# Performance work log

Hardware: AMD Instinct MI355X
Metric: run time of the kernel (lower is better)

The kernel has to match this reference:

```python
import jax, jax.numpy as jnp
import numpy as np
import math

B, S, D, H = 4, 2048, 1024, 16
DK = D // H
DFF = 1024  # FeedForward default d_ff=1024 (DecoderLayer passes only d_model)
EPS = 1e-6
SQRT_2_OVER_PI = math.sqrt(2.0 / math.pi)


def setup_inputs() -> dict:
    key = jax.random.key(0)
    ks = jax.random.split(key, 12)
    sc = 0.02
    x = jax.random.normal(ks[0], (B, S, D), dtype=jnp.float32)
    # causal look-ahead mask: 1 where attendable, 0 where masked
    mask = jnp.broadcast_to(jnp.tril(jnp.ones((S, S), dtype=jnp.int32)), (B, S, S))
    inp = {
        'x': x,
        'mask': mask,
        'Wq': jax.random.normal(ks[1], (D, D), jnp.float32) * sc,
        'bq': jnp.zeros((D,), jnp.float32),
        'Wk': jax.random.normal(ks[2], (D, D), jnp.float32) * sc,
        'bk': jnp.zeros((D,), jnp.float32),
        'Wv': jax.random.normal(ks[3], (D, D), jnp.float32) * sc,
        'bv': jnp.zeros((D,), jnp.float32),
        'Wo': jax.random.normal(ks[4], (D, D), jnp.float32) * sc,
        'bo': jnp.zeros((D,), jnp.float32),
        'W1': jax.random.normal(ks[5], (D, DFF), jnp.float32) * sc,
        'b1': jnp.zeros((DFF,), jnp.float32),
        'W2': jax.random.normal(ks[6], (DFF, D), jnp.float32) * sc,
        'b2': jnp.zeros((D,), jnp.float32),
        'alpha1': jnp.ones((D,), jnp.float32),
        'bias1': jnp.zeros((D,), jnp.float32),
        'alpha2': jnp.ones((D,), jnp.float32),
        'bias2': jnp.zeros((D,), jnp.float32),
    }
    return inp


def _norm(x, alpha, bias):
    # torch: (x - mean) / (x.std(unbiased=True) + eps) * alpha + bias
    mean = jnp.mean(x, axis=-1, keepdims=True)
    var = jnp.sum((x - mean) ** 2, axis=-1, keepdims=True) / (x.shape[-1] - 1)
    std = jnp.sqrt(var)
    return alpha * (x - mean) / (std + EPS) + bias


def _gelu(x):
    return 0.5 * x * (1.0 + jnp.tanh(SQRT_2_OVER_PI * (x + 0.044715 * x ** 3)))


def reference(x, mask, Wq, bq, Wk, bk, Wv, bv, Wo, bo, W1, b1, W2, b2,
              alpha1, bias1, alpha2, bias2):
    b, s, d = x.shape
    x2 = _norm(x, alpha1, bias1)
    q = (x2 @ Wq + bq).reshape(b, s, H, DK).transpose(0, 2, 1, 3)  # bhsd
    k = (x2 @ Wk + bk).reshape(b, s, H, DK).transpose(0, 2, 1, 3)
    v = (x2 @ Wv + bv).reshape(b, s, H, DK).transpose(0, 2, 1, 3)
    scores = jnp.einsum('bhqd,bhkd->bhqk', q, k) / jnp.sqrt(jnp.float32(DK))
    scores = jnp.where(mask[:, None, :, :] == 0, jnp.float32(-1e9), scores)
    probs = jax.nn.softmax(scores, axis=-1)
    attn = jnp.einsum('bhqk,bhkd->bhqd', probs, v)
    concat = attn.transpose(0, 2, 1, 3).reshape(b, s, d)
    x = x + (concat @ Wo + bo)
    x2 = _norm(x, alpha2, bias2)
    ff = _gelu(x2 @ W1 + b1) @ W2 + b2
    return x + ff
```

## Files before the change

### kernel.cpp

```cpp
#include <hip/hip_runtime.h>
#include <hip/hip_bf16.h>
#include <math.h>


#define B_ 4
#define S_ 2048
#define D_ 1024
#define H_ 16
#define DFF_ 1024

typedef __attribute__((ext_vector_type(8))) short short8;
typedef __attribute__((ext_vector_type(8))) unsigned short ushort8;
typedef __attribute__((ext_vector_type(4))) float f32x4;

__device__ __forceinline__ unsigned short f2bf(float f) {
  __hip_bfloat16 h = __float2bfloat16(f);
  return *reinterpret_cast<unsigned short*>(&h);
}

__device__ __forceinline__ void gload16(const void* g, void* l) {
  __builtin_amdgcn_global_load_lds(
      (const __attribute__((address_space(1))) void*)g,
      (__attribute__((address_space(3))) void*)l, 16, 0, 0);
}

__global__ __launch_bounds__(256) void tcast6_k(
    const float* s0, const float* s1, const float* s2, const float* s3,
    const float* s4, const float* s5, unsigned short* d0, unsigned short* d1,
    unsigned short* d2, unsigned short* d3, unsigned short* d4,
    unsigned short* d5) {
  const float* src;
  unsigned short* dst;
  switch (blockIdx.z) {
    case 0: src = s0; dst = d0; break;
    case 1: src = s1; dst = d1; break;
    case 2: src = s2; dst = d2; break;
    case 3: src = s3; dst = d3; break;
    case 4: src = s4; dst = d4; break;
    default: src = s5; dst = d5; break;
  }
  __shared__ float tile[64][65];
  const int k0 = blockIdx.y * 64, n0 = blockIdx.x * 64;
  const int t = threadIdx.x;
  const int r = t >> 2, c0 = (t & 3) * 16;
  const float4* sp =
      reinterpret_cast<const float4*>(src + (size_t)(k0 + r) * 1024 + n0 + c0);
#pragma unroll
  for (int j = 0; j < 4; ++j) {
    float4 v = sp[j];
    tile[r][c0 + 4 * j] = v.x;
    tile[r][c0 + 4 * j + 1] = v.y;
    tile[r][c0 + 4 * j + 2] = v.z;
    tile[r][c0 + 4 * j + 3] = v.w;
  }
  __syncthreads();
  ushort8 o0, o1;
#pragma unroll
  for (int j = 0; j < 8; ++j) o0[j] = f2bf(tile[c0 + j][r]);
#pragma unroll
  for (int j = 0; j < 8; ++j) o1[j] = f2bf(tile[c0 + 8 + j][r]);
  unsigned short* dp = dst + (size_t)(n0 + r) * 1024 + k0 + c0;
  *reinterpret_cast<ushort8*>(dp) = o0;
  *reinterpret_cast<ushort8*>(dp + 8) = o1;
}

__global__ __launch_bounds__(256) void ln_k(const float* __restrict__ x,
                                            const float* __restrict__ alpha,
                                            const float* __restrict__ bias,
                                            unsigned short* __restrict__ out) {
  int row = blockIdx.x, t = threadIdx.x;
  float4 v = reinterpret_cast<const float4*>(x + (size_t)row * D_)[t];
  float s = v.x + v.y + v.z + v.w;
  float q = v.x * v.x + v.y * v.y + v.z * v.z + v.w * v.w;
#pragma unroll
  for (int off = 32; off > 0; off >>= 1) {
    s += __shfl_down(s, off);
    q += __shfl_down(q, off);
  }
  __shared__ float ss[4], sq[4], stat[2];
  if ((t & 63) == 0) { ss[t >> 6] = s; sq[t >> 6] = q; }
  __syncthreads();
  if (t == 0) {
    float S = ss[0] + ss[1] + ss[2] + ss[3];
    float Q = sq[0] + sq[1] + sq[2] + sq[3];
    float mean = S * (1.0f / D_);
    float var = fmaxf((Q - D_ * mean * mean) * (1.0f / (D_ - 1)), 0.0f);
    stat[0] = mean;
    stat[1] = 1.0f / (sqrtf(var) + 1e-6f);
  }
  __syncthreads();
  float mean = stat[0], inv = stat[1];
  float4 a = reinterpret_cast<const float4*>(alpha)[t];
  float4 b = reinterpret_cast<const float4*>(bias)[t];
  ushort4 o;
  o.x = f2bf((v.x - mean) * inv * a.x + b.x);
  o.y = f2bf((v.y - mean) * inv * a.y + b.y);
  o.z = f2bf((v.z - mean) * inv * a.z + b.z);
  o.w = f2bf((v.w - mean) * inv * a.w + b.w);
  reinterpret_cast<ushort4*>(out + (size_t)row * D_)[t] = o;
}

__device__ __forceinline__ void gemm_core64(
    const unsigned short* __restrict__ A, const unsigned short* __restrict__ Wt,
    int m0, int n0, int K, unsigned short* As ,
    unsigned short* Bs , f32x4 (&acc)[2][4]) {
  const int t = threadIdx.x;
  const int wv = t >> 6, lane = t & 63, quad = lane >> 4, l16 = lane & 15;
  const int wm = wv >> 1, wn = wv & 1;
  const int lr8 = lane >> 3;
  const int lseg = ((lane & 7) ^ lr8) * 8;

  const unsigned short* Ag0 = A + (size_t)(m0 + wv * 16 + lr8) * K + lseg;
  const unsigned short* Ag1 = A + (size_t)(m0 + wv * 16 + 8 + lr8) * K + lseg;
  const unsigned short* Bg0 = Wt + (size_t)(n0 + wv * 32 + lr8) * K + lseg;
  const unsigned short* Bg1 = Wt + (size_t)(n0 + wv * 32 + 8 + lr8) * K + lseg;
  const unsigned short* Bg2 = Wt + (size_t)(n0 + wv * 32 + 16 + lr8) * K + lseg;
  const unsigned short* Bg3 = Wt + (size_t)(n0 + wv * 32 + 24 + lr8) * K + lseg;
  unsigned short* Al0 = &As[(wv * 16) * 64];
  unsigned short* Al1 = &As[(wv * 16 + 8) * 64];
  unsigned short* Bl0 = &Bs[(wv * 32) * 64];
  unsigned short* Bl1 = &Bs[(wv * 32 + 8) * 64];
  unsigned short* Bl2 = &Bs[(wv * 32 + 16) * 64];
  unsigned short* Bl3 = &Bs[(wv * 32 + 24) * 64];

  for (int k0 = 0; k0 < K; k0 += 64) {
    gload16(Ag0, Al0);
    gload16(Ag1, Al1);
    gload16(Bg0, Bl0);
    gload16(Bg1, Bl1);
    gload16(Bg2, Bl2);
    gload16(Bg3, Bl3);
    __syncthreads();
    short8 af[2][2], bf[2][4];
#pragma unroll
    for (int p = 0; p < 2; ++p) {
#pragma unroll
      for (int mt = 0; mt < 2; ++mt) {
        int r = wm * 32 + mt * 16 + l16;
        af[p][mt] = *reinterpret_cast<const short8*>(
            &As[r * 64 + (((p * 4 + quad) ^ (r & 7)) << 3)]);
      }
#pragma unroll
      for (int nt = 0; nt < 4; ++nt) {
        int r = wn * 64 + nt * 16 + l16;
        bf[p][nt] = *reinterpret_cast<const short8*>(
            &Bs[r * 64 + (((p * 4 + quad) ^ (r & 7)) << 3)]);
      }
    }
#pragma unroll
    for (int p = 0; p < 2; ++p)
#pragma unroll
      for (int mt = 0; mt < 2; ++mt)
#pragma unroll
        for (int nt = 0; nt < 4; ++nt)
          acc[mt][nt] = __builtin_amdgcn_mfma_f32_16x16x32_bf16(
              af[p][mt], bf[p][nt], acc[mt][nt], 0, 0, 0);
    __syncthreads();
    Ag0 += 64; Ag1 += 64; Bg0 += 64; Bg1 += 64; Bg2 += 64; Bg3 += 64;
  }
}

__global__ __launch_bounds__(256, 4) void gemm_k(
    const unsigned short* __restrict__ A, const unsigned short* __restrict__ Wt,
    const float* __restrict__ bias, const float* __restrict__ res,
    void* __restrict__ outp, int M, int N, int K, int flags) {
  __shared__ unsigned short As[64 * 64];
  __shared__ unsigned short Bs[128 * 64];
  const int t = threadIdx.x;
  const int m0 = blockIdx.y * 64, n0 = blockIdx.x * 128;
  const int wv = t >> 6, lane = t & 63, quad = lane >> 4, l16 = lane & 15;
  const int wm = wv >> 1, wn = wv & 1;
  f32x4 acc[2][4] = {};
  gemm_core64(A, Wt, m0, n0, K, As, Bs, acc);

  const bool obf = flags & 1, dog = flags & 2;
#pragma unroll
  for (int nt = 0; nt < 4; ++nt) {
    int col = n0 + wn * 64 + nt * 16 + l16;
    float bv = bias[col];
#pragma unroll
    for (int mt = 0; mt < 2; ++mt) {
#pragma unroll
      for (int r = 0; r < 4; ++r) {
        int row = m0 + wm * 32 + mt * 16 + quad * 4 + r;
        float v = acc[mt][nt][r] + bv;
        if (res) v += res[(size_t)row * N + col];
        if (dog) {
          float e = __expf(1.5957691216057308f * (v + 0.044715f * v * v * v));
          float th = 1.0f - 2.0f / (1.0f + e);
          v = 0.5f * v * (1.0f + th);
        }
        if (obf)
          ((unsigned short*)outp)[(size_t)row * N + col] = f2bf(v);
        else
          ((float*)outp)[(size_t)row * N + col] = v;
      }
    }
  }
}

__global__ __launch_bounds__(256, 4) void gemmqkv_k(
    const unsigned short* __restrict__ A, const unsigned short* __restrict__ Wt,
    const float* __restrict__ bq, const float* __restrict__ bk,
    const float* __restrict__ bv, unsigned short* __restrict__ outq,
    unsigned short* __restrict__ outk, unsigned short* __restrict__ outvt,
    int M, int K) {
  __shared__ unsigned short As[64 * 64];
  __shared__ unsigned short Bs[128 * 64];
  const int t = threadIdx.x;
  const int m0 = blockIdx.y * 64, n0 = blockIdx.x * 128;
  const int wv = t >> 6, lane = t & 63, quad = lane >> 4, l16 = lane & 15;
  const int wm = wv >> 1, wn = wv & 1;
  f32x4 acc[2][4] = {};
  gemm_core64(A, Wt, m0, n0, K, As, Bs, acc);

  const int seg = n0 >> 10;
  const int nb = n0 & 1023;
  const float* bias = (seg == 0) ? bq : (seg == 1) ? bk : bv;
  if (seg < 2) {
    unsigned short* o = (seg == 0) ? outq : outk;
#pragma unroll
    for (int nt = 0; nt < 4; ++nt) {
      int col = nb + wn * 64 + nt * 16 + l16;
      float bvv = bias[col];
#pragma unroll
      for (int mt = 0; mt < 2; ++mt)
#pragma unroll
        for (int r = 0; r < 4; ++r) {
          int row = m0 + wm * 32 + mt * 16 + quad * 4 + r;
          o[(size_t)row * D_ + col] = f2bf(acc[mt][nt][r] + bvv);
        }
    }
  } else {
#pragma unroll
    for (int nt = 0; nt < 4; ++nt) {
      int col = nb + wn * 64 + nt * 16 + l16;
      float bvv = bias[col];
      int h = col >> 6, dk = col & 63;
#pragma unroll
      for (int mt = 0; mt < 2; ++mt) {
        int m = m0 + wm * 32 + mt * 16 + quad * 4;
        int b = m >> 11, sidx = m & 2047;
        ushort4 o;
        o.x = f2bf(acc[mt][nt][0] + bvv);
        o.y = f2bf(acc[mt][nt][1] + bvv);
        o.z = f2bf(acc[mt][nt][2] + bvv);
        o.w = f2bf(acc[mt][nt][3] + bvv);
        *reinterpret_cast<ushort4*>(
            &outvt[(((size_t)(b * 16 + h) * 64 + dk) * 2048 + sidx)]) = o;
      }
    }
  }
}

__global__ __launch_bounds__(256, 2) void attn_k(
    const unsigned short* __restrict__ Q, const unsigned short* __restrict__ Kg,
    const unsigned short* __restrict__ VT, unsigned short* __restrict__ Og) {
  __shared__ unsigned short Ks[64 * 64];
  __shared__ unsigned short Vs[64 * 64];
  __shared__ unsigned short Ps[4 * 32 * 72];
  const int t = threadIdx.x;
  const int pair = blockIdx.x >> 6, bh = blockIdx.x & 63;
  const int b = bh >> 4, h = bh & 15;
  const int hi = 31 - pair, lo = pair;
  const int w = t >> 6, lane = t & 63, quad = lane >> 4, l16 = lane & 15;
  const int qhi0 = hi * 64 + w * 16, qlo0 = lo * 64 + w * 16;
  unsigned short* PsW = &Ps[w * 32 * 72];

  short8 qfh[2], qfl[2];
#pragma unroll
  for (int kc = 0; kc < 2; ++kc) {
    qfh[kc] = *reinterpret_cast<const short8*>(
        Q + (size_t)(b * S_ + qhi0 + l16) * D_ + h * 64 + kc * 32 + quad * 8);
    qfl[kc] = *reinterpret_cast<const short8*>(
        Q + (size_t)(b * S_ + qlo0 + l16) * D_ + h * 64 + kc * 32 + quad * 8);
  }
  f32x4 Oh[4] = {}, Ol[4] = {};
  float lh_acc = 0.0f, ll_acc = 0.0f;

  const int srA = w * 8 + (lane >> 3);
  const int ssA = ((lane & 7) ^ (srA & 7)) * 8;
  const int srB = srA + 32;
  const int ssB = ((lane & 7) ^ (srB & 7)) * 8;
  const unsigned short* KgA = Kg + (size_t)(b * S_ + srA) * D_ + h * 64 + ssA;
  const unsigned short* KgB = Kg + (size_t)(b * S_ + srB) * D_ + h * 64 + ssB;
  const unsigned short* VgA = VT + ((size_t)bh * 64 + srA) * 2048 + ssA;
  const unsigned short* VgB = VT + ((size_t)bh * 64 + srB) * 2048 + ssB;
  unsigned short* KlA = &Ks[(w * 8) * 64];
  unsigned short* KlB = &Ks[(32 + w * 8) * 64];
  unsigned short* VlA = &Vs[(w * 8) * 64];
  unsigned short* VlB = &Vs[(32 + w * 8) * 64];

  const float C0 = 0.18033688011f;
  const float C1 = -23.08312065f;

  for (int kt = 0; kt <= hi; ++kt) {
    const int k0 = kt * 64;
    const bool dolo = (kt <= lo);

    gload16(KgA, KlA);
    gload16(KgB, KlB);
    gload16(VgA, VlA);
    gload16(VgB, VlB);
    __syncthreads();

    f32x4 sch[4] = {}, scl[4] = {};
#pragma unroll
    for (int mt = 0; mt < 4; ++mt) {
      int r = mt * 16 + l16;
      short8 kf0 = *reinterpret_cast<const short8*>(
          &Ks[r * 64 + ((quad ^ (r & 7)) << 3)]);
      short8 kf1 = *reinterpret_cast<const short8*>(
          &Ks[r * 64 + (((4 + quad) ^ (r & 7)) << 3)]);
      sch[mt] = __builtin_amdgcn_mfma_f32_16x16x32_bf16(kf0, qfh[0], sch[mt],
                                                        0, 0, 0);
      sch[mt] = __builtin_amdgcn_mfma_f32_16x16x32_bf16(kf1, qfh[1], sch[mt],
                                                        0, 0, 0);
      if (dolo) {
        scl[mt] = __builtin_amdgcn_mfma_f32_16x16x32_bf16(kf0, qfl[0], scl[mt],
                                                          0, 0, 0);
        scl[mt] = __builtin_amdgcn_mfma_f32_16x16x32_bf16(kf1, qfl[1], scl[mt],
                                                          0, 0, 0);
      }
    }

    {
      const bool diag = (kt == hi);
      const int q = qhi0 + l16;
#pragma unroll
      for (int mt = 0; mt < 4; ++mt) {
        float pv[4];
#pragma unroll
        for (int r = 0; r < 4; ++r) {
          int key = k0 + mt * 16 + quad * 4 + r;
          float p = __builtin_amdgcn_exp2f(fmaf(sch[mt][r], C0, C1));
          if (diag && key > q) p = 0.0f;
          lh_acc += p;
          pv[r] = p;
        }
        ushort4 pk = {f2bf(pv[0]), f2bf(pv[1]), f2bf(pv[2]), f2bf(pv[3])};
        *reinterpret_cast<ushort4*>(&PsW[l16 * 72 + mt * 16 + quad * 4]) = pk;
      }
    }
    if (dolo) {
      const bool diag = (kt == lo);
      const int q = qlo0 + l16;
#pragma unroll
      for (int mt = 0; mt < 4; ++mt) {
        float pv[4];
#pragma unroll
        for (int r = 0; r < 4; ++r) {
          int key = k0 + mt * 16 + quad * 4 + r;
          float p = __builtin_amdgcn_exp2f(fmaf(scl[mt][r], C0, C1));
          if (diag && key > q) p = 0.0f;
          ll_acc += p;
          pv[r] = p;
        }
        ushort4 pk = {f2bf(pv[0]), f2bf(pv[1]), f2bf(pv[2]), f2bf(pv[3])};
        *reinterpret_cast<ushort4*>(
            &PsW[(16 + l16) * 72 + mt * 16 + quad * 4]) = pk;
      }
    }
    __builtin_amdgcn_sched_barrier(0);

    short8 pfh[2], pfl[2];
#pragma unroll
    for (int kc = 0; kc < 2; ++kc)
      pfh[kc] = *reinterpret_cast<const short8*>(
          &PsW[l16 * 72 + kc * 32 + quad * 8]);
    if (dolo) {
#pragma unroll
      for (int kc = 0; kc < 2; ++kc)
        pfl[kc] = *reinterpret_cast<const short8*>(
            &PsW[(16 + l16) * 72 + kc * 32 + quad * 8]);
    }

#pragma unroll
    for (int kc = 0; kc < 2; ++kc) {
#pragma unroll
      for (int nd = 0; nd < 4; ++nd) {
        int r = nd * 16 + l16;
        short8 vf = *reinterpret_cast<const short8*>(
            &Vs[r * 64 + (((kc * 4 + quad) ^ (r & 7)) << 3)]);
        Oh[nd] = __builtin_amdgcn_mfma_f32_16x16x32_bf16(pfh[kc], vf, Oh[nd],
                                                         0, 0, 0);
        if (dolo)
          Ol[nd] = __builtin_amdgcn_mfma_f32_16x16x32_bf16(pfl[kc], vf, Ol[nd],
                                                           0, 0, 0);
      }
    }
    __syncthreads();
    KgA += (size_t)64 * D_;
    KgB += (size_t)64 * D_;
    VgA += 64;
    VgB += 64;
  }

  lh_acc += __shfl_xor(lh_acc, 16);
  lh_acc += __shfl_xor(lh_acc, 32);
  ll_acc += __shfl_xor(ll_acc, 16);
  ll_acc += __shfl_xor(ll_acc, 32);

#pragma unroll
  for (int r = 0; r < 4; ++r) {
    float lh = __shfl(lh_acc, quad * 4 + r);
    float ll = __shfl(ll_acc, quad * 4 + r);
    float rlh = 1.0f / lh, rll = 1.0f / ll;
#pragma unroll
    for (int nd = 0; nd < 4; ++nd) {
      Og[(size_t)(b * S_ + qhi0 + quad * 4 + r) * D_ + h * 64 + nd * 16 + l16] =
          f2bf(Oh[nd][r] * rlh);
      Og[(size_t)(b * S_ + qlo0 + quad * 4 + r) * D_ + h * 64 + nd * 16 + l16] =
          f2bf(Ol[nd][r] * rll);
    }
  }
}

extern "C" void kernel_launch(void* const* d_in, const int* in_sizes, int n_in,
                              void* d_out, int out_size, void* d_ws,
                              size_t ws_size, hipStream_t stream) {
  const float* x = (const float*)d_in[0];
  const float* Wq = (const float*)d_in[2];
  const float* bq = (const float*)d_in[3];
  const float* Wk = (const float*)d_in[4];
  const float* bk = (const float*)d_in[5];
  const float* Wv = (const float*)d_in[6];
  const float* bv = (const float*)d_in[7];
  const float* Wo = (const float*)d_in[8];
  const float* bo = (const float*)d_in[9];
  const float* W1 = (const float*)d_in[10];
  const float* b1 = (const float*)d_in[11];
  const float* W2 = (const float*)d_in[12];
  const float* b2 = (const float*)d_in[13];
  const float* alpha1 = (const float*)d_in[14];
  const float* bias1 = (const float*)d_in[15];
  const float* alpha2 = (const float*)d_in[16];
  const float* bias2 = (const float*)d_in[17];
  float* out = (float*)d_out;

  char* ws = (char*)d_ws;
  const size_t MB = 1024 * 1024;
  unsigned short* wqT = (unsigned short*)(ws + 0 * MB);
  unsigned short* wkT = (unsigned short*)(ws + 2 * MB);
  unsigned short* wvT = (unsigned short*)(ws + 4 * MB);
  unsigned short* woT = (unsigned short*)(ws + 6 * MB);
  unsigned short* w1T = (unsigned short*)(ws + 8 * MB);
  unsigned short* w2T = (unsigned short*)(ws + 10 * MB);
  unsigned short* x2a = (unsigned short*)(ws + 12 * MB);
  unsigned short* qb = (unsigned short*)(ws + 28 * MB);
  unsigned short* kb = (unsigned short*)(ws + 44 * MB);
  unsigned short* vtb = (unsigned short*)(ws + 60 * MB);

  tcast6_k<<<dim3(16, 16, 6), dim3(256), 0, stream>>>(Wq, Wk, Wv, Wo, W1, W2,
                                                      wqT, wkT, wvT, woT, w1T,
                                                      w2T);

  const int M = B_ * S_;
  ln_k<<<dim3(M), dim3(256), 0, stream>>>(x, alpha1, bias1, x2a);

  gemmqkv_k<<<dim3(24, 128), dim3(256), 0, stream>>>(x2a, wqT, bq, bk, bv, qb,
                                                     kb, vtb, M, D_);

  attn_k<<<dim3(1024), dim3(256), 0, stream>>>(qb, kb, vtb, x2a);

  dim3 gg(D_ / 128, M / 64);
  gemm_k<<<gg, dim3(256), 0, stream>>>(x2a, woT, bo, x, out, M, D_, D_, 0);

  ln_k<<<dim3(M), dim3(256), 0, stream>>>(out, alpha2, bias2, qb);

  gemm_k<<<gg, dim3(256), 0, stream>>>(qb, w1T, b1, nullptr, kb, M, DFF_, D_, 3);

  gemm_k<<<gg, dim3(256), 0, stream>>>(kb, w2T, b2, out, out, M, D_, DFF_, 0);
}
```

Before: 420.5 us.

## Double-buffer K/V tiles in attention kernel with async prefetch

Doubles the LDS K and V tile buffers and issues the global-to-LDS loads for the next key tile before computing on the current one. Explicit vmcnt waits and raw barriers replace the per-iteration __syncthreads, so memory latency can overlap the MFMA and softmax work. This doubles LDS use for K/V, which may affect occupancy at 2 blocks per CU. It also relies on hand-written waitcnt counts being correct with respect to the other outstanding loads.

```diff
diff --git a/kernel.cpp b/kernel.cpp
--- a/kernel.cpp
+++ b/kernel.cpp
@@ -256,8 +256,8 @@
 __global__ __launch_bounds__(256, 2) void attn_k(
     const unsigned short* __restrict__ Q, const unsigned short* __restrict__ Kg,
     const unsigned short* __restrict__ VT, unsigned short* __restrict__ Og) {
-  __shared__ unsigned short Ks[64 * 64];
-  __shared__ unsigned short Vs[64 * 64];
+  __shared__ unsigned short Ks[2][64 * 64];
+  __shared__ unsigned short Vs[2][64 * 64];
   __shared__ unsigned short Ps[4 * 32 * 72];
   const int t = threadIdx.x;
   const int pair = blockIdx.x >> 6, bh = blockIdx.x & 63;
@@ -275,6 +275,9 @@
     qfl[kc] = *reinterpret_cast<const short8*>(
         Q + (size_t)(b * S_ + qlo0 + l16) * D_ + h * 64 + kc * 32 + quad * 8);
   }
+  asm volatile("" ::"v"(qfh[0]), "v"(qfh[1]), "v"(qfl[0]), "v"(qfl[1])
+               : "memory");
+
   f32x4 Oh[4] = {}, Ol[4] = {};
   float lh_acc = 0.0f, ll_acc = 0.0f;
 
@@ -286,32 +289,55 @@
   const unsigned short* KgB = Kg + (size_t)(b * S_ + srB) * D_ + h * 64 + ssB;
   const unsigned short* VgA = VT + ((size_t)bh * 64 + srA) * 2048 + ssA;
   const unsigned short* VgB = VT + ((size_t)bh * 64 + srB) * 2048 + ssB;
-  unsigned short* KlA = &Ks[(w * 8) * 64];
-  unsigned short* KlB = &Ks[(32 + w * 8) * 64];
-  unsigned short* VlA = &Vs[(w * 8) * 64];
-  unsigned short* VlB = &Vs[(32 + w * 8) * 64];
+  unsigned short* KlA = &Ks[0][(w * 8) * 64];
+  unsigned short* KlB = &Ks[0][(32 + w * 8) * 64];
+  unsigned short* VlA = &Vs[0][(w * 8) * 64];
+  unsigned short* VlB = &Vs[0][(32 + w * 8) * 64];
 
   const float C0 = 0.18033688011f;
   const float C1 = -23.08312065f;
+
+  gload16(KgA, KlA);
+  gload16(KgB, KlB);
+  gload16(VgA, VlA);
+  gload16(VgB, VlB);
+  KgA += (size_t)64 * D_;
+  KgB += (size_t)64 * D_;
+  VgA += 64;
+  VgB += 64;
 
   for (int kt = 0; kt <= hi; ++kt) {
     const int k0 = kt * 64;
     const bool dolo = (kt <= lo);
-
-    gload16(KgA, KlA);
-    gload16(KgB, KlB);
-    gload16(VgA, VlA);
-    gload16(VgB, VlB);
-    __syncthreads();
+    const int coff = (kt & 1) << 12;
+    const int noff = ((kt & 1) ^ 1) << 12;
+
+    if (kt < hi) {
+      gload16(KgA, KlA + noff);
+      gload16(KgB, KlB + noff);
+      gload16(VgA, VlA + noff);
+      gload16(VgB, VlB + noff);
+      KgA += (size_t)64 * D_;
+      KgB += (size_t)64 * D_;
+      VgA += 64;
+      VgB += 64;
+      asm volatile("s_waitcnt vmcnt(4)" ::: "memory");
+    } else {
+      asm volatile("s_waitcnt vmcnt(0)" ::: "memory");
+    }
+    asm volatile("s_barrier" ::: "memory");
+
+    const unsigned short* Ksc = &Ks[0][coff];
+    const unsigned short* Vsc = &Vs[0][coff];
 
     f32x4 sch[4] = {}, scl[4] = {};
 #pragma unroll
     for (int mt = 0; mt < 4; ++mt) {
       int r = mt * 16 + l16;
       short8 kf0 = *reinterpret_cast<const short8*>(
-          &Ks[r * 64 + ((quad ^ (r & 7)) << 3)]);
+          &Ksc[r * 64 + ((quad ^ (r & 7)) << 3)]);
       short8 kf1 = *reinterpret_cast<const short8*>(
-          &Ks[r * 64 + (((4 + quad) ^ (r & 7)) << 3)]);
+          &Ksc[r * 64 + (((4 + quad) ^ (r & 7)) << 3)]);
       sch[mt] = __builtin_amdgcn_mfma_f32_16x16x32_bf16(kf0, qfh[0], sch[mt],
                                                         0, 0, 0);
       sch[mt] = __builtin_amdgcn_mfma_f32_16x16x32_bf16(kf1, qfh[1], sch[mt],
@@ -381,7 +407,7 @@
       for (int nd = 0; nd < 4; ++nd) {
         int r = nd * 16 + l16;
         short8 vf = *reinterpret_cast<const short8*>(
-            &Vs[r * 64 + (((kc * 4 + quad) ^ (r & 7)) << 3)]);
+            &Vsc[r * 64 + (((kc * 4 + quad) ^ (r & 7)) << 3)]);
         Oh[nd] = __builtin_amdgcn_mfma_f32_16x16x32_bf16(pfh[kc], vf, Oh[nd],
                                                          0, 0, 0);
         if (dolo)
@@ -389,11 +415,7 @@
                                                            0, 0, 0);
       }
     }
-    __syncthreads();
-    KgA += (size_t)64 * D_;
-    KgB += (size_t)64 * D_;
-    VgA += 64;
-    VgB += 64;
+    asm volatile("s_barrier" ::: "memory");
   }
 
   lh_acc += __shfl_xor(lh_acc, 16);
```

Measured after the change: 429.8 us. 1.02x slower.
